# Performance work log

Hardware: AMD Instinct MI355X
Metric: run time of the kernel (lower is better)

Reference implementation:

```python
import jax, jax.numpy as jnp
import numpy as np

N, D, S, C = 2048, 1024, 49, 1000


def setup_inputs() -> dict:
    key = jax.random.key(0)
    k1, k2, k3 = jax.random.split(key, 3)
    x = jax.random.normal(k1, (N, D, S), dtype=jnp.float32)
    mu = jax.random.normal(k2, (C, D), dtype=jnp.float32)
    # precision = inverse covariance -> symmetric PSD; build a well-conditioned one
    R = jax.random.normal(k3, (D, D), dtype=jnp.float32)
    precision = (R @ R.T) / D + jnp.eye(D, dtype=jnp.float32)
    return {"x": x, "mu": mu, "precision": precision}


def reference(x, mu, precision):
    # z: [N, D] global-average-pooled features (z.view(N, D, -1).mean(2))
    z = jnp.mean(x, axis=2)
    # score[n, c] = -0.5 * (z_n - mu_c) @ P @ (z_n - mu_c)
    # Expanded to avoid materializing [N, C, D]:
    #   zPz - z P mu - mu P z + mu P mu   (no symmetry assumption on P)
    zP = z @ precision                      # [N, D]
    zPt = z @ precision.T                   # [N, D]
    qz = jnp.sum(zP * z, axis=1)            # [N]   diag(z P z^T)
    cross1 = zP @ mu.T                      # [N, C] z P mu
    cross2 = zPt @ mu.T                     # [N, C] mu P z
    qmu = jnp.einsum('cd,de,ce->c', mu, precision, mu)  # [C]
    score = -0.5 * (qz[:, None] - cross1 - cross2 + qmu[None, :])
    return score
```

## Files before the change

### kernel.cpp

```cpp
#include <hip/hip_runtime.h>
#include <hip/hip_bf16.h>

typedef unsigned short u16;
typedef __bf16 bf16x8 __attribute__((ext_vector_type(8)));
typedef float f32x4 __attribute__((ext_vector_type(4)));

typedef const __attribute__((address_space(1))) void gv_t;
typedef __attribute__((address_space(3))) void lv_t;

#define NN 2048
#define DD 1024
#define SS 49
#define CC 1000
#define CP 1024

#define BK 64
#define KK DD
#define NT (KK / BK)

__device__ inline u16 f2bf(float f) {
    __hip_bfloat16 h = __float2bfloat16(f);
    union { __hip_bfloat16 h; u16 u; } cv; cv.h = h; return cv.u;
}

__device__ __forceinline__ void gemm64_core(const u16* __restrict__ A,
                                            const u16* __restrict__ Bt,
                                            int m0, int n0, char* smem,
                                            f32x4 acc[2][2], int tid) {
    char* As = smem;
    char* Bs = smem + 16384;
    const int lane = tid & 63;
    const int wr = (tid >> 6) >> 1, wc = (tid >> 6) & 1;
    const int r16 = lane & 15, hk = lane >> 4;
    const char* Ab = (const char*)A;
    const char* Bb = (const char*)Bt;

    auto stage = [&](int buf, int k0) {
        #pragma unroll
        for (int j = 0; j < 2; j++) {
            const int c = j * 256 + tid;
            const int row = c >> 3, slot = c & 7;
            const int goff = ((slot ^ (row & 7)) << 4);
            __builtin_amdgcn_global_load_lds(
                (gv_t*)(Ab + ((size_t)(m0 + row) * KK + k0) * 2 + goff),
                (lv_t*)(As + buf * 8192 + c * 16), 16, 0, 0);
            __builtin_amdgcn_global_load_lds(
                (gv_t*)(Bb + ((size_t)(n0 + row) * KK + k0) * 2 + goff),
                (lv_t*)(Bs + buf * 8192 + c * 16), 16, 0, 0);
        }
    };

    stage(0, 0);
    __syncthreads();
    int cur = 0;
    for (int t = 0; t < NT; ++t) {
        if (t + 1 < NT) stage(cur ^ 1, (t + 1) * BK);
        bf16x8 a[2][2], b[2][2];
        #pragma unroll
        for (int mi = 0; mi < 2; mi++) {
            const int row = wr * 32 + mi * 16 + r16;
            #pragma unroll
            for (int kk2 = 0; kk2 < 2; kk2++) {
                const int g = kk2 * 4 + hk;
                a[mi][kk2] = *(const bf16x8*)(As + cur * 8192 + row * 128 + ((g ^ (row & 7)) << 4));
            }
        }
        #pragma unroll
        for (int ni = 0; ni < 2; ni++) {
            const int row = wc * 32 + ni * 16 + r16;
            #pragma unroll
            for (int kk2 = 0; kk2 < 2; kk2++) {
                const int g = kk2 * 4 + hk;
                b[ni][kk2] = *(const bf16x8*)(Bs + cur * 8192 + row * 128 + ((g ^ (row & 7)) << 4));
            }
        }
        #pragma unroll
        for (int kk2 = 0; kk2 < 2; kk2++)
            #pragma unroll
            for (int mi = 0; mi < 2; mi++)
                #pragma unroll
                for (int ni = 0; ni < 2; ni++)
                    acc[mi][ni] = __builtin_amdgcn_mfma_f32_16x16x32_bf16(
                        a[mi][kk2], b[ni][kk2], acc[mi][ni], 0, 0, 0);
        __syncthreads();
        cur ^= 1;
    }
}

__global__ __launch_bounds__(256) void prep_k(const float* __restrict__ P,
                                              const float* __restrict__ mu,
                                              u16* __restrict__ q,
                                              u16* __restrict__ mu_bf,
                                              float* __restrict__ qzh,
                                              float* __restrict__ qmuh) {
    __shared__ float t1[64][65];
    __shared__ float t2[64][65];
    const int tid = threadIdx.x, bid = blockIdx.x;
    const int br = bid >> 4, bc = bid & 15;
    const int br64 = br * 64, bc64 = bc * 64;

    #pragma unroll
    for (int it = 0; it < 16; it++) {
        const int idx = it * 256 + tid;
        const int row = idx >> 6, col = idx & 63;
        t1[row][col] = P[(size_t)(br64 + row) * DD + bc64 + col];
        t2[row][col] = P[(size_t)(bc64 + row) * DD + br64 + col];
    }
    __syncthreads();
    #pragma unroll
    for (int it = 0; it < 16; it++) {
        const int idx = it * 256 + tid;
        const int row = idx >> 6, col = idx & 63;
        q[(size_t)(br64 + row) * DD + bc64 + col] = f2bf(t1[row][col] + t2[col][row]);
    }

    const size_t base = (size_t)bid * 4096;
    #pragma unroll
    for (int it = 0; it < 16; it++) {
        const size_t j = base + it * 256 + tid;
        const int r = (int)(j >> 10);
        mu_bf[j] = f2bf(r < CC ? mu[j] : 0.f);
    }
    const int g = bid * 256 + tid;
    if (g < NN) qzh[g]  = 0.f;
    if (g < CP) qmuh[g] = 0.f;
}

__global__ __launch_bounds__(256) void pool_muq_k(const float* __restrict__ x,
                                                  const u16* __restrict__ q,
                                                  const u16* __restrict__ mu_bf,
                                                  const float* __restrict__ mu,
                                                  u16* __restrict__ b_bf,
                                                  float* __restrict__ qmuh,
                                                  float* __restrict__ zf,
                                                  u16* __restrict__ zb) {
    __shared__ char smem[50176];
    const int tid = threadIdx.x;
    const int bid = blockIdx.x;

    if (bid >= 256) {
        const int u = bid - 256;
        float* lds = (float*)smem;
        const size_t base = (size_t)u * (256 * SS);
        const float4* src = (const float4*)(x + base);
        float4* dst = (float4*)lds;
        #pragma unroll
        for (int i = 0; i < 13; i++) {
            int idx = i * 256 + tid;
            if (idx < (256 * SS) / 4) dst[idx] = src[idx];
        }
        __syncthreads();
        const float* r = lds + tid * SS;
        float s = 0.f;
        #pragma unroll
        for (int j = 0; j < SS; j++) s += r[j];
        s *= (1.f / 49.f);
        size_t o = (size_t)u * 256 + tid;
        zf[o] = s;
        zb[o] = f2bf(s);
        return;
    }

    const int m0 = (bid >> 4) * 64, n0 = (bid & 15) * 64;
    f32x4 acc[2][2] = {};
    gemm64_core(mu_bf, q, m0, n0, smem, acc, tid);

    const int lane = tid & 63;
    const int wr = (tid >> 6) >> 1, wc = (tid >> 6) & 1;
    const int cr = (lane >> 4) * 4, cc2 = lane & 15;
    #pragma unroll
    for (int mi = 0; mi < 2; mi++) {
        const int gr0 = m0 + wr * 32 + mi * 16 + cr;
        #pragma unroll
        for (int r = 0; r < 4; r++) {
            const int row = gr0 + r;
            float v = 0.f;
            #pragma unroll
            for (int ni = 0; ni < 2; ni++) {
                const int gc = n0 + wc * 32 + ni * 16 + cc2;
                float av = acc[mi][ni][r];
                float sv = (row < CC) ? mu[(size_t)row * DD + gc] : 0.f;
                v += av * sv;
                b_bf[(size_t)row * DD + gc] = f2bf(av);
            }
            #pragma unroll
            for (int m = 1; m < 16; m <<= 1) v += __shfl_xor(v, m);
            if (cc2 == 0) atomicAdd(qmuh + row, 0.25f * v);
        }
    }
}

__global__ __launch_bounds__(256) void zscore_k(const u16* __restrict__ z_bf,
                                                const u16* __restrict__ q,
                                                const u16* __restrict__ b_bf,
                                                const float* __restrict__ zf,
                                                float* __restrict__ qzh,
                                                const float* __restrict__ qmuh,
                                                float* __restrict__ out) {
    __shared__ char smem[49152];
    const int tid = threadIdx.x, bid = blockIdx.x;
    const int m0 = (bid >> 4) * 64, n0 = (bid & 15) * 64;
    const int lane = tid & 63;
    const int wr = (tid >> 6) >> 1, wc = (tid >> 6) & 1;
    const int r16 = lane & 15, hk = lane >> 4;
    char* As = smem;
    char* Bq = smem + 16384;
    char* Bb = smem + 32768;
    const char* Ap = (const char*)z_bf;
    const char* Qp = (const char*)q;
    const char* Bp = (const char*)b_bf;

    f32x4 accS[2][2] = {};
    f32x4 accZ[2][2] = {};

    auto stage = [&](int buf, int k0) {
        #pragma unroll
        for (int j = 0; j < 2; j++) {
            const int c = j * 256 + tid;
            const int row = c >> 3, slot = c & 7;
            const int goff = ((slot ^ (row & 7)) << 4);
            const size_t ao = ((size_t)(m0 + row) * KK + k0) * 2 + goff;
            const size_t bo = ((size_t)(n0 + row) * KK + k0) * 2 + goff;
            __builtin_amdgcn_global_load_lds((gv_t*)(Ap + ao),
                (lv_t*)(As + buf * 8192 + c * 16), 16, 0, 0);
            __builtin_amdgcn_global_load_lds((gv_t*)(Qp + bo),
                (lv_t*)(Bq + buf * 8192 + c * 16), 16, 0, 0);
            __builtin_amdgcn_global_load_lds((gv_t*)(Bp + bo),
                (lv_t*)(Bb + buf * 8192 + c * 16), 16, 0, 0);
        }
    };

    stage(0, 0);
    __syncthreads();
    int cur = 0;
    for (int t = 0; t < NT; ++t) {
        if (t + 1 < NT) stage(cur ^ 1, (t + 1) * BK);
        bf16x8 a[2][2], bq[2][2], bb[2][2];
        #pragma unroll
        for (int mi = 0; mi < 2; mi++) {
            const int row = wr * 32 + mi * 16 + r16;
            #pragma unroll
            for (int kk2 = 0; kk2 < 2; kk2++) {
                const int g = kk2 * 4 + hk;
                a[mi][kk2] = *(const bf16x8*)(As + cur * 8192 + row * 128 + ((g ^ (row & 7)) << 4));
            }
        }
        #pragma unroll
        for (int ni = 0; ni < 2; ni++) {
            const int row = wc * 32 + ni * 16 + r16;
            #pragma unroll
            for (int kk2 = 0; kk2 < 2; kk2++) {
                const int g = kk2 * 4 + hk;
                const int off = row * 128 + ((g ^ (row & 7)) << 4);
                bq[ni][kk2] = *(const bf16x8*)(Bq + cur * 8192 + off);
                bb[ni][kk2] = *(const bf16x8*)(Bb + cur * 8192 + off);
            }
        }
        #pragma unroll
        for (int kk2 = 0; kk2 < 2; kk2++)
            #pragma unroll
            for (int mi = 0; mi < 2; mi++)
                #pragma unroll
                for (int ni = 0; ni < 2; ni++) {
                    accS[mi][ni] = __builtin_amdgcn_mfma_f32_16x16x32_bf16(
                        a[mi][kk2], bb[ni][kk2], accS[mi][ni], 0, 0, 0);
                    accZ[mi][ni] = __builtin_amdgcn_mfma_f32_16x16x32_bf16(
                        a[mi][kk2], bq[ni][kk2], accZ[mi][ni], 0, 0, 0);
                }
        __syncthreads();
        cur ^= 1;
    }

    const int cr = hk * 4, cc2 = r16;
    #pragma unroll
    for (int mi = 0; mi < 2; mi++) {
        const int gr0 = m0 + wr * 32 + mi * 16 + cr;
        #pragma unroll
        for (int r = 0; r < 4; r++) {
            const int row = gr0 + r;
            float v = 0.f;
            #pragma unroll
            for (int ni = 0; ni < 2; ni++) {
                const int gc = n0 + wc * 32 + ni * 16 + cc2;
                v += accZ[mi][ni][r] * zf[(size_t)row * DD + gc];
            }
            #pragma unroll
            for (int m = 1; m < 16; m <<= 1) v += __shfl_xor(v, m);
            if (cc2 == 0) atomicAdd(qzh + row, 0.25f * v);
        }
    }
    #pragma unroll
    for (int mi = 0; mi < 2; mi++) {
        #pragma unroll
        for (int ni = 0; ni < 2; ni++) {
            const int gr = m0 + wr * 32 + mi * 16 + cr;
            const int gc = n0 + wc * 32 + ni * 16 + cc2;
            if (gc < CC) {
                const float qm = qmuh[gc];
                #pragma unroll
                for (int r = 0; r < 4; r++)
                    out[(size_t)(gr + r) * CC + gc] =
                        0.5f * accS[mi][ni][r] - qm;
            }
        }
    }
}

__global__ __launch_bounds__(256) void fixup_k(float* __restrict__ out,
                                               const float* __restrict__ qzh) {
    const int n = blockIdx.x, tid = threadIdx.x;
    if (tid >= 250) return;
    const float qz = qzh[n];
    float4* p = (float4*)(out + (size_t)n * CC + tid * 4);
    float4 v = *p;
    v.x -= qz; v.y -= qz; v.z -= qz; v.w -= qz;
    *p = v;
}

extern "C" void kernel_launch(void* const* d_in, const int* in_sizes, int n_in,
                              void* d_out, int out_size, void* d_ws, size_t ws_size,
                              hipStream_t stream) {
    const float* x  = (const float*)d_in[0];
    const float* mu = (const float*)d_in[1];
    const float* P  = (const float*)d_in[2];
    float* out = (float*)d_out;

    char* w = (char*)d_ws;
    u16*   q_bf  = (u16*)w;   w += (size_t)DD * DD * 2;
    u16*   mu_bf = (u16*)w;   w += (size_t)CP * DD * 2;
    u16*   b_bf  = (u16*)w;   w += (size_t)CP * DD * 2;
    u16*   z_bf  = (u16*)w;   w += (size_t)NN * DD * 2;
    float* zf    = (float*)w; w += (size_t)NN * DD * 4;
    float* qzh   = (float*)w; w += (size_t)NN * 4;
    float* qmuh  = (float*)w;

    prep_k<<<256, 256, 0, stream>>>(P, mu, q_bf, mu_bf, qzh, qmuh);
    pool_muq_k<<<256 + (NN * DD) / 256, 256, 0, stream>>>(
        x, q_bf, mu_bf, mu, b_bf, qmuh, zf, z_bf);
    zscore_k<<<512, 256, 0, stream>>>(z_bf, q_bf, b_bf, zf, qzh, qmuh, out);
    fixup_k<<<NN, 256, 0, stream>>>(out, qzh);
}
```

Before: 120.6 us.

## Fuse all four stages into one persistent cooperative kernel with grid syncs

Replaces the four separate launches (prep, pool/mu-Q GEMM, score GEMM, qz fixup) with one cooperatively launched persistent kernel. Each stage is a device function that the blocks loop over in grid-stride fashion, and stages are separated by threadfence plus grid.sync. The goal is to remove kernel launch gaps and tail effects between stages. In exchange, the grid is capped at the occupancy-limited block count, so the bandwidth-bound pooling stage has fewer blocks in flight. Each grid-wide barrier also adds its own synchronization cost.

```diff
diff --git a/kernel.cpp b/kernel.cpp
--- a/kernel.cpp
+++ b/kernel.cpp
@@ -1,5 +1,8 @@
 #include <hip/hip_runtime.h>
 #include <hip/hip_bf16.h>
+#include <hip/hip_cooperative_groups.h>
+
+namespace cg = cooperative_groups;
 
 typedef unsigned short u16;
 typedef __bf16 bf16x8 __attribute__((ext_vector_type(8)));
@@ -87,16 +90,15 @@
     }
 }
 
-__global__ __launch_bounds__(256) void prep_k(const float* __restrict__ P,
-                                              const float* __restrict__ mu,
-                                              u16* __restrict__ q,
-                                              u16* __restrict__ mu_bf,
-                                              float* __restrict__ qzh,
-                                              float* __restrict__ qmuh) {
-    __shared__ float t1[64][65];
-    __shared__ float t2[64][65];
-    const int tid = threadIdx.x, bid = blockIdx.x;
-    const int br = bid >> 4, bc = bid & 15;
+
+__device__ __forceinline__ void prep_tile(int t, const float* __restrict__ P,
+                                          const float* __restrict__ mu,
+                                          u16* __restrict__ q,
+                                          u16* __restrict__ mu_bf,
+                                          char* smem, int tid) {
+    float (*t1)[65] = (float(*)[65])smem;
+    float (*t2)[65] = (float(*)[65])(smem + 16640);
+    const int br = t >> 4, bc = t & 15;
     const int br64 = br * 64, bc64 = bc * 64;
 
     #pragma unroll
@@ -113,55 +115,48 @@
         const int row = idx >> 6, col = idx & 63;
         q[(size_t)(br64 + row) * DD + bc64 + col] = f2bf(t1[row][col] + t2[col][row]);
     }
-
-    const size_t base = (size_t)bid * 4096;
+    const size_t base = (size_t)t * 4096;
     #pragma unroll
     for (int it = 0; it < 16; it++) {
         const size_t j = base + it * 256 + tid;
         const int r = (int)(j >> 10);
         mu_bf[j] = f2bf(r < CC ? mu[j] : 0.f);
     }
-    const int g = bid * 256 + tid;
-    if (g < NN) qzh[g]  = 0.f;
-    if (g < CP) qmuh[g] = 0.f;
-}
-
-__global__ __launch_bounds__(256) void pool_muq_k(const float* __restrict__ x,
-                                                  const u16* __restrict__ q,
-                                                  const u16* __restrict__ mu_bf,
-                                                  const float* __restrict__ mu,
-                                                  u16* __restrict__ b_bf,
-                                                  float* __restrict__ qmuh,
-                                                  float* __restrict__ zf,
-                                                  u16* __restrict__ zb) {
-    __shared__ char smem[50176];
-    const int tid = threadIdx.x;
-    const int bid = blockIdx.x;
-
-    if (bid >= 256) {
-        const int u = bid - 256;
-        float* lds = (float*)smem;
-        const size_t base = (size_t)u * (256 * SS);
-        const float4* src = (const float4*)(x + base);
-        float4* dst = (float4*)lds;
-        #pragma unroll
-        for (int i = 0; i < 13; i++) {
-            int idx = i * 256 + tid;
-            if (idx < (256 * SS) / 4) dst[idx] = src[idx];
-        }
-        __syncthreads();
-        const float* r = lds + tid * SS;
-        float s = 0.f;
-        #pragma unroll
-        for (int j = 0; j < SS; j++) s += r[j];
-        s *= (1.f / 49.f);
-        size_t o = (size_t)u * 256 + tid;
-        zf[o] = s;
-        zb[o] = f2bf(s);
-        return;
-    }
-
-    const int m0 = (bid >> 4) * 64, n0 = (bid & 15) * 64;
+    __syncthreads();
+}
+
+__device__ __forceinline__ void pool_unit(int u, const float* __restrict__ x,
+                                          float* __restrict__ zf,
+                                          u16* __restrict__ zb,
+                                          char* smem, int tid) {
+    float* lds = (float*)smem;
+    const size_t base = (size_t)u * (256 * SS);
+    const float4* src = (const float4*)(x + base);
+    float4* dst = (float4*)lds;
+    #pragma unroll
+    for (int i = 0; i < 13; i++) {
+        int idx = i * 256 + tid;
+        if (idx < (256 * SS) / 4) dst[idx] = src[idx];
+    }
+    __syncthreads();
+    const float* r = lds + tid * SS;
+    float s = 0.f;
+    #pragma unroll
+    for (int j = 0; j < SS; j++) s += r[j];
+    s *= (1.f / 49.f);
+    size_t o = (size_t)u * 256 + tid;
+    zf[o] = s;
+    zb[o] = f2bf(s);
+    __syncthreads();
+}
+
+__device__ __forceinline__ void muq_tile(int t, const u16* __restrict__ mu_bf,
+                                         const u16* __restrict__ q,
+                                         const float* __restrict__ mu,
+                                         u16* __restrict__ b_bf,
+                                         float* __restrict__ qmuh,
+                                         char* smem, int tid) {
+    const int m0 = (t >> 4) * 64, n0 = (t & 15) * 64;
     f32x4 acc[2][2] = {};
     gemm64_core(mu_bf, q, m0, n0, smem, acc, tid);
 
@@ -190,16 +185,15 @@
     }
 }
 
-__global__ __launch_bounds__(256) void zscore_k(const u16* __restrict__ z_bf,
-                                                const u16* __restrict__ q,
-                                                const u16* __restrict__ b_bf,
-                                                const float* __restrict__ zf,
-                                                float* __restrict__ qzh,
-                                                const float* __restrict__ qmuh,
-                                                float* __restrict__ out) {
-    __shared__ char smem[49152];
-    const int tid = threadIdx.x, bid = blockIdx.x;
-    const int m0 = (bid >> 4) * 64, n0 = (bid & 15) * 64;
+__device__ __forceinline__ void zscore_tile(int t, const u16* __restrict__ z_bf,
+                                            const u16* __restrict__ q,
+                                            const u16* __restrict__ b_bf,
+                                            const float* __restrict__ zf,
+                                            float* __restrict__ qzh,
+                                            const float* __restrict__ qmuh,
+                                            float* __restrict__ out,
+                                            char* smem, int tid) {
+    const int m0 = (t >> 4) * 64, n0 = (t & 15) * 64;
     const int lane = tid & 63;
     const int wr = (tid >> 6) >> 1, wc = (tid >> 6) & 1;
     const int r16 = lane & 15, hk = lane >> 4;
@@ -233,8 +227,8 @@
     stage(0, 0);
     __syncthreads();
     int cur = 0;
-    for (int t = 0; t < NT; ++t) {
-        if (t + 1 < NT) stage(cur ^ 1, (t + 1) * BK);
+    for (int kt = 0; kt < NT; ++kt) {
+        if (kt + 1 < NT) stage(cur ^ 1, (kt + 1) * BK);
         bf16x8 a[2][2], bq[2][2], bb[2][2];
         #pragma unroll
         for (int mi = 0; mi < 2; mi++) {
@@ -306,15 +300,52 @@
     }
 }
 
-__global__ __launch_bounds__(256) void fixup_k(float* __restrict__ out,
-                                               const float* __restrict__ qzh) {
-    const int n = blockIdx.x, tid = threadIdx.x;
-    if (tid >= 250) return;
-    const float qz = qzh[n];
-    float4* p = (float4*)(out + (size_t)n * CC + tid * 4);
-    float4 v = *p;
-    v.x -= qz; v.y -= qz; v.z -= qz; v.w -= qz;
-    *p = v;
+__global__ __launch_bounds__(256) void mega_k(const float* __restrict__ x,
+                                              const float* __restrict__ P,
+                                              const float* __restrict__ mu,
+                                              u16* __restrict__ q,
+                                              u16* __restrict__ mu_bf,
+                                              u16* __restrict__ b_bf,
+                                              u16* __restrict__ z_bf,
+                                              float* __restrict__ zf,
+                                              float* __restrict__ qzh,
+                                              float* __restrict__ qmuh,
+                                              float* __restrict__ out) {
+    cg::grid_group grid = cg::this_grid();
+    __shared__ char smem[50176];
+    const int tid = threadIdx.x, bid = blockIdx.x, NB = gridDim.x;
+
+    {
+        const int g = bid * 256 + tid;
+        if (g < NN) qzh[g]  = 0.f;
+        if (g < CP) qmuh[g] = 0.f;
+    }
+    for (int t = bid; t < 256; t += NB)
+        prep_tile(t, P, mu, q, mu_bf, smem, tid);
+    __threadfence();
+    grid.sync();
+
+    for (int i = bid; i < 256 + 8192; i += NB) {
+        if (i < 256) muq_tile(i, mu_bf, q, mu, b_bf, qmuh, smem, tid);
+        else         pool_unit(i - 256, x, zf, z_bf, smem, tid);
+    }
+    __threadfence();
+    grid.sync();
+
+    for (int t = bid; t < 512; t += NB)
+        zscore_tile(t, z_bf, q, b_bf, zf, qzh, qmuh, out, smem, tid);
+    __threadfence();
+    grid.sync();
+
+    for (int n = bid; n < NN; n += NB) {
+        if (tid < 250) {
+            const float qz = qzh[n];
+            float4* p = (float4*)(out + (size_t)n * CC + tid * 4);
+            float4 v = *p;
+            v.x -= qz; v.y -= qz; v.z -= qz; v.w -= qz;
+            *p = v;
+        }
+    }
 }
 
 extern "C" void kernel_launch(void* const* d_in, const int* in_sizes, int n_in,
@@ -334,9 +365,16 @@
     float* qzh   = (float*)w; w += (size_t)NN * 4;
     float* qmuh  = (float*)w;
 
-    prep_k<<<256, 256, 0, stream>>>(P, mu, q_bf, mu_bf, qzh, qmuh);
-    pool_muq_k<<<256 + (NN * DD) / 256, 256, 0, stream>>>(
-        x, q_bf, mu_bf, mu, b_bf, qmuh, zf, z_bf);
-    zscore_k<<<512, 256, 0, stream>>>(z_bf, q_bf, b_bf, zf, qzh, qmuh, out);
-    fixup_k<<<NN, 256, 0, stream>>>(out, qzh);
-}
+    int occ = 0;
+    if (hipOccupancyMaxActiveBlocksPerMultiprocessor(&occ, (const void*)mega_k,
+                                                     256, 0) != hipSuccess || occ < 1)
+        occ = 1;
+    int NB = occ * 256;
+    if (NB > 768) NB = 768;
+
+    void* args[] = { (void*)&x, (void*)&P, (void*)&mu, (void*)&q_bf,
+                     (void*)&mu_bf, (void*)&b_bf, (void*)&z_bf, (void*)&zf,
+                     (void*)&qzh, (void*)&qmuh, (void*)&out };
+    hipLaunchCooperativeKernel((const void*)mega_k, dim3(NB), dim3(256),
+                               args, 0, stream);
+}
```

Measured after the change: 363.0 us. 3.01x slower.
